# Kernel tuning notes

Hardware: AMD Instinct MI355X
Metric: run time of the kernel (lower is better)

## Reference

```python
import jax, jax.numpy as jnp
import numpy as np
from jax import lax

B, T, H, W = 1, 8, 28, 28
DIM, NH = 768, 12
HD = DIM // NH
N = 1 + T * H * W
SCALE = HD ** -0.5
STRIDE_KV = (1, 2, 2)
EPS = 1e-5


def setup_inputs():
    key = jax.random.key(0)
    ks = jax.random.split(key, 8)
    f = jax.random.normal
    return {
        "x": f(ks[0], (B, N, DIM), jnp.float32),
        "qkv_w": f(ks[1], (3 * DIM, DIM), jnp.float32) * 0.02,
        "qkv_b": jnp.zeros((3 * DIM,), jnp.float32),
        "proj_w": f(ks[2], (DIM, DIM), jnp.float32) * 0.02,
        "proj_b": jnp.zeros((DIM,), jnp.float32),
        "pool_k_w": f(ks[3], (HD, 1, 3, 3, 3), jnp.float32) * 0.1,
        "pool_v_w": f(ks[4], (HD, 1, 3, 3, 3), jnp.float32) * 0.1,
        "norm_k_g": jnp.ones((HD,), jnp.float32),
        "norm_k_b": jnp.zeros((HD,), jnp.float32),
        "norm_v_g": jnp.ones((HD,), jnp.float32),
        "norm_v_b": jnp.zeros((HD,), jnp.float32),
        "rel_pos_h": f(ks[5], (2 * H - 1, HD), jnp.float32) * 0.02,
        "rel_pos_w": f(ks[6], (2 * W - 1, HD), jnp.float32) * 0.02,
        "rel_pos_t": f(ks[7], (2 * T - 1, HD), jnp.float32) * 0.02,
    }


def _rel_idx(qn, kn):
    # static relative-distance index table (matches cal_rel_pos_* in torch)
    qr = max(kn / qn, 1.0)
    kr = max(qn / kn, 1.0)
    d = np.arange(qn)[:, None] * qr - np.arange(kn)[None, :] * kr + (kn - 1) * kr
    return d.astype(np.int32)


def _layernorm(y, g, b):
    mu = y.mean(-1, keepdims=True)
    var = ((y - mu) ** 2).mean(-1, keepdims=True)
    return (y - mu) * lax.rsqrt(var + EPS) * g + b


def _pool(t, wker, g, b):
    # t: (B, NH, N, HD); depthwise Conv3d pooling on non-cls tokens, then LN
    cls_tok, rest = t[:, :, :1], t[:, :, 1:]
    xr = rest.reshape(B * NH, T, H, W, HD)
    ker = jnp.transpose(wker, (2, 3, 4, 1, 0))  # (kT,kH,kW,1,HD)
    y = lax.conv_general_dilated(
        xr, ker, window_strides=STRIDE_KV, padding=[(1, 1), (1, 1), (1, 1)],
        dimension_numbers=("NDHWC", "DHWIO", "NDHWC"), feature_group_count=HD)
    kt, kh, kw = y.shape[1:4]
    y = y.reshape(B, NH, kt * kh * kw, HD)
    y = jnp.concatenate([cls_tok, y], axis=2)
    return _layernorm(y, g, b), (kt, kh, kw)


def reference(x, qkv_w, qkv_b, proj_w, proj_b, pool_k_w, pool_v_w,
              norm_k_g, norm_k_b, norm_v_g, norm_v_b,
              rel_pos_h, rel_pos_w, rel_pos_t):
    qkv = (x @ qkv_w.T + qkv_b).reshape(B, N, 3, NH, HD)
    qkv = jnp.transpose(qkv, (2, 0, 3, 1, 4))  # (3, B, NH, N, HD)
    q, k, v = qkv[0], qkv[1], qkv[2]
    k, (kt, kh, kw) = _pool(k, pool_k_w, norm_k_g, norm_k_b)
    v, _ = _pool(v, pool_v_w, norm_v_g, norm_v_b)

    attn = jnp.einsum("bhqc,bhkc->bhqk", q * SCALE, k)  # (B,NH,N,1+kt*kh*kw)

    # decomposed relative position bias (spatial h/w + temporal), cls excluded
    r_q = q[:, :, 1:].reshape(B, NH, T, H, W, HD)
    Rh = rel_pos_h[_rel_idx(H, kh)]  # (H, kh, HD)
    Rw = rel_pos_w[_rel_idx(W, kw)]  # (W, kw, HD)
    Rt = rel_pos_t[_rel_idx(T, kt)]  # (T, kt, HD)
    rel_h = jnp.einsum("bnthwc,hkc->bnthwk", r_q, Rh)
    rel_w = jnp.einsum("bnthwc,wkc->bnthwk", r_q, Rw)
    rel_t = jnp.einsum("bnthwc,tkc->bnthwk", r_q, Rt)
    bias = (rel_h[:, :, :, :, :, None, :, None]
            + rel_w[:, :, :, :, :, None, None, :]
            + rel_t[:, :, :, :, :, :, None, None])
    a_sp = attn[:, :, 1:, 1:].reshape(B, NH, T, H, W, kt, kh, kw) + bias
    attn = attn.at[:, :, 1:, 1:].set(a_sp.reshape(B, NH, T * H * W, kt * kh * kw))

    attn = jax.nn.softmax(attn, axis=-1)
    out = jnp.einsum("bhqk,bhkc->bhqc", attn, v)
    out = out.transpose(0, 2, 1, 3).reshape(B, N, DIM)
    return out @ proj_w.T + proj_b
```

## Files before the change

### kernel.cpp

```cpp
#include <hip/hip_runtime.h>

#define N_Q   6273
#define N_KEY 1569
#define NHEAD 12
#define HD    64
#define DQH   128
#define DIMM  768
#define NSP   6272
#define SCALE 0.125f
#define LOG2E 1.44269504f
#define QSC   (SCALE * LOG2E)
#define EPSLN 1e-5f
#define DEFER_THR 11.5f

typedef __bf16 bf16x8 __attribute__((ext_vector_type(8)));
typedef float  f32x4  __attribute__((ext_vector_type(4)));
typedef unsigned short ushort_t;
typedef unsigned int uint_t;

__device__ __forceinline__ ushort_t f2bf(float f) {
    union { float f; unsigned u; } v; v.f = f;
    unsigned r = (v.u + 0x7FFFu + ((v.u >> 16) & 1u)) >> 16;
    return (ushort_t)r;
}
__device__ __forceinline__ float bf2f(ushort_t b) {
    union { unsigned u; float f; } v; v.u = ((unsigned)b) << 16;
    return v.f;
}
__device__ __forceinline__ ushort_t cvt_native(float f) {
    __bf16 h = (__bf16)f;
    return *(ushort_t*)&h;
}
__device__ __forceinline__ uint_t pk2(float a, float b) {
    return (uint_t)cvt_native(a) | ((uint_t)cvt_native(b) << 16);
}
__device__ __forceinline__ void gload_lds16(const ushort_t* g, ushort_t* l) {
    __builtin_amdgcn_global_load_lds(
        (const __attribute__((address_space(1))) void*)g,
        (__attribute__((address_space(3))) void*)l, 16, 0, 0);
}
__device__ __forceinline__ int xcd_swz(int orig, int nwg) {
    int xcd = orig & 7, j = orig >> 3;
    int q = nwg >> 3, r = nwg & 7;
    return (xcd < r ? xcd * (q + 1) : r * (q + 1) + (xcd - r) * q) + j;
}

__global__ __launch_bounds__(256) void cvt3_bf16(
    const float* __restrict__ s0, const float* __restrict__ s1,
    const float* __restrict__ s2, ushort_t* __restrict__ dst,
    int n0, int n1, int n2)
{
    int total = n0 + n1 + n2;
    int stride = gridDim.x * 256;
    for (int i = blockIdx.x * 256 + threadIdx.x; i < total; i += stride) {
        const float* src; int j;
        if (i < n0)           { src = s0; j = i; }
        else if (i < n0 + n1) { src = s1; j = i - n0; }
        else                  { src = s2; j = i - n0 - n1; }
        const float4* s4 = (const float4*)src + (size_t)j * 2;
        float4 a = s4[0], b = s4[1];
        uint4 o;
        o.x = (unsigned)f2bf(a.x) | ((unsigned)f2bf(a.y) << 16);
        o.y = (unsigned)f2bf(a.z) | ((unsigned)f2bf(a.w) << 16);
        o.z = (unsigned)f2bf(b.x) | ((unsigned)f2bf(b.y) << 16);
        o.w = (unsigned)f2bf(b.z) | ((unsigned)f2bf(b.w) << 16);
        *(uint4*)&dst[(size_t)i * 8] = o;
    }
}

template <int MODE>
__global__ __launch_bounds__(512) void gemm_pipe(
    const ushort_t* __restrict__ A, const ushort_t* __restrict__ B,
    const float* __restrict__ bias, int M,
    float* __restrict__ Cf, ushort_t* __restrict__ qd, ushort_t* __restrict__ kd,
    ushort_t* __restrict__ vd)
{
    __shared__ ushort_t sm[32768];
    const int tid = threadIdx.x;
    const int wave = tid >> 6, lane = tid & 63;
    const int lo = lane & 15, hi = lane >> 4;
    const int nbx = gridDim.x;
    const int lin = xcd_swz(blockIdx.x + blockIdx.y * nbx, nbx * gridDim.y);
    const int bx = lin % nbx, by = lin / nbx;
    const int row0 = by * 128, col0 = bx * 128;
    const int wr = wave >> 2;
    const int wc = wave & 3;
    const int K = DIMM;
    const int NT = K / 64;

    f32x4 acc[4][2];
#pragma unroll
    for (int i = 0; i < 4; ++i)
#pragma unroll
        for (int j = 0; j < 2; ++j)
#pragma unroll
            for (int r = 0; r < 4; ++r) acc[i][j][r] = 0.f;

    const int sr = lane >> 3;
    const int scb = (lane & 7) * 16;

    auto stage = [&](int t) {
        ushort_t* Ab = sm + ((t & 1) ? 16384 : 0);
        ushort_t* Bb = Ab + 8192;
        const int k0 = t * 64;
#pragma unroll
        for (int i = 0; i < 2; ++i) {
            int ch = wave * 2 + i;
            int r = ch * 8 + sr;
            int cbs = scb ^ ((r & 7) << 4);
            int ga = row0 + r; if (ga > M - 1) ga = M - 1;
            gload_lds16(&A[(size_t)ga * K + k0 + (cbs >> 1)], &Ab[ch * 512]);
            gload_lds16(&B[(size_t)(col0 + r) * K + k0 + (cbs >> 1)], &Bb[ch * 512]);
        }
    };

    stage(0);
    for (int t = 0; t < NT; ++t) {
        __syncthreads();
        if (t + 1 < NT) stage(t + 1);
        ushort_t* Ab = sm + ((t & 1) ? 16384 : 0);
        ushort_t* Bb = Ab + 8192;
#pragma unroll
        for (int ks = 0; ks < 2; ++ks) {
            bf16x8 af[4], bfr[2];
#pragma unroll
            for (int s = 0; s < 4; ++s) {
                int ra = wr * 64 + s * 16 + lo;
                int ca = (ks * 64 + hi * 16) ^ ((ra & 7) << 4);
                af[s] = *(const bf16x8*)&Ab[ra * 64 + (ca >> 1)];
            }
#pragma unroll
            for (int s2 = 0; s2 < 2; ++s2) {
                int rb = wc * 32 + s2 * 16 + lo;
                int cb2 = (ks * 64 + hi * 16) ^ ((rb & 7) << 4);
                bfr[s2] = *(const bf16x8*)&Bb[rb * 64 + (cb2 >> 1)];
            }
#pragma unroll
            for (int i = 0; i < 4; ++i)
#pragma unroll
                for (int j = 0; j < 2; ++j)
                    acc[i][j] = __builtin_amdgcn_mfma_f32_16x16x32_bf16(
                        af[i], bfr[j], acc[i][j], 0, 0, 0);
        }
    }

#pragma unroll
    for (int i = 0; i < 4; ++i) {
#pragma unroll
        for (int reg = 0; reg < 4; ++reg) {
            int r = row0 + wr * 64 + i * 16 + hi * 4 + reg;
            if (r >= M) continue;
#pragma unroll
            for (int j = 0; j < 2; ++j) {
                int c = col0 + wc * 32 + j * 16 + lo;
                float val = acc[i][j][reg] + bias[c];
                if (MODE == 0) {
                    Cf[(size_t)r * DIMM + c] = val;
                } else {
                    int which = c / DIMM;
                    int rem = c - which * DIMM;
                    int head = rem >> 6, d = rem & 63;
                    if (which == 0) {
                        qd[((size_t)head * N_Q + r) * DQH + d] = f2bf(val * QSC);
                    } else {
                        ushort_t* dst = (which == 1) ? kd : vd;
                        dst[((size_t)head * N_Q + r) * HD + d] = f2bf(val);
                    }
                }
            }
        }
    }
}

__global__ __launch_bounds__(256) void pool_ln2(
    const ushort_t* __restrict__ kin, const ushort_t* __restrict__ vin,
    const float* __restrict__ wkk, const float* __restrict__ wkv,
    const float* __restrict__ gk, const float* __restrict__ bk,
    const float* __restrict__ gv, const float* __restrict__ bv,
    ushort_t* __restrict__ kout, ushort_t* __restrict__ vout)
{
    const int is_k = (blockIdx.y == 0);
    const ushort_t* in = is_k ? kin : vin;
    const float* wk = is_k ? wkk : wkv;
    const float* g  = is_k ? gk : gv;
    const float* b  = is_k ? bk : bv;

    __shared__ float ws_s[27][64];
    const int tid = threadIdx.x;
    for (int e = tid; e < 27 * 64; e += 256) {
        int d = e / 27, tap = e - d * 27;
        ws_s[tap][d] = wk[e];
    }
    __syncthreads();

    const int wave = tid >> 6, lane = tid & 63;
    const float gl = g[lane], bl = b[lane];

#pragma unroll 1
    for (int p4 = 0; p4 < 4; ++p4) {
        const int pos = (blockIdx.x * 4 + wave) * 4 + p4;
        if (pos >= NHEAD * N_KEY) continue;
        const int head = pos / N_KEY;
        const int idx = pos - head * N_KEY;
        const ushort_t* base = in + (size_t)head * N_Q * HD;

        float val;
        if (idx == 0) {
            val = bf2f(base[lane]);
        } else {
            int p = idx - 1;
            int t1 = p / 196;
            int h1 = (p / 14) % 14;
            int w1 = p % 14;
            val = 0.f;
            if (t1 >= 1 && t1 <= 6 && h1 >= 1 && w1 >= 1) {
                int n0 = 1 + ((t1 - 1) * 28 + (2 * h1 - 1)) * 28 + (2 * w1 - 1);
#pragma unroll
                for (int dt = 0; dt < 3; ++dt)
#pragma unroll
                    for (int dh = 0; dh < 3; ++dh)
#pragma unroll
                        for (int dw = 0; dw < 3; ++dw) {
                            int n = n0 + (dt * 784) + (dh * 28) + dw;
                            val += bf2f(base[(size_t)n * HD + lane]) *
                                   ws_s[(dt * 3 + dh) * 3 + dw][lane];
                        }
            } else {
#pragma unroll
                for (int dt = 0; dt < 3; ++dt) {
                    int t = t1 + dt - 1;
                    if (t < 0 || t >= 8) continue;
#pragma unroll
                    for (int dh = 0; dh < 3; ++dh) {
                        int h = 2 * h1 + dh - 1;
                        if (h < 0 || h >= 28) continue;
#pragma unroll
                        for (int dw = 0; dw < 3; ++dw) {
                            int w = 2 * w1 + dw - 1;
                            if (w < 0 || w >= 28) continue;
                            int n = 1 + (t * 28 + h) * 28 + w;
                            val += bf2f(base[(size_t)n * HD + lane]) *
                                   ws_s[(dt * 3 + dh) * 3 + dw][lane];
                        }
                    }
                }
            }
        }
        float mu = val;
#pragma unroll
        for (int off = 1; off < 64; off <<= 1) mu += __shfl_xor(mu, off, 64);
        mu *= (1.f / 64.f);
        float dv = val - mu;
        float var = dv * dv;
#pragma unroll
        for (int off = 1; off < 64; off <<= 1) var += __shfl_xor(var, off, 64);
        var *= (1.f / 64.f);
        float ln = dv * rsqrtf(var + EPSLN) * gl + bl;

        if (!is_k) {
            vout[(size_t)pos * HD + lane] = f2bf(ln);
        } else {
            kout[(size_t)pos * DQH + lane] = f2bf(ln);
            float oh = 0.f;
            if (idx > 0) {
                int p = idx - 1;
                int kt = p / 196, kh = (p / 14) % 14, kw = p % 14;
                if ((lane < 14 && lane == kh) ||
                    (lane >= 14 && lane < 28 && (lane - 14) == kw) ||
                    (lane >= 28 && lane < 36 && (lane - 28) == kt))
                    oh = 1.f;
            }
            kout[(size_t)pos * DQH + 64 + lane] = f2bf(oh);
        }
    }
}

__global__ __launch_bounds__(256) void rel_gemm(
    ushort_t* __restrict__ qhat, const float* __restrict__ rh,
    const float* __restrict__ rw, const float* __restrict__ rt)
{
    __shared__ ushort_t sm[17408];
    const int tid = threadIdx.x;
    const int wave = tid >> 6, lane = tid & 63;
    const int lo = lane & 15, hi = lane >> 4;
    const int head = blockIdx.y;

    if (blockIdx.x == 49) {
        if (tid < 64) qhat[((size_t)head * N_Q) * DQH + 64 + tid] = 0;
        return;
    }
    const int qs0 = blockIdx.x * 128;
    ushort_t* Al = sm;
    ushort_t* Bl = sm + 8192;

    const int sr = lane >> 3;
    const int scb = (lane & 7) * 16;
#pragma unroll
    for (int i = 0; i < 4; ++i) {
        int ch = wave * 4 + i;
        int rl = ch * 8 + sr;
        int cbs = scb ^ ((rl & 7) << 4);
        gload_lds16(&qhat[((size_t)head * N_Q + 1 + qs0 + rl) * DQH + (cbs >> 1)],
                    &Al[ch * 512]);
    }
#pragma unroll
    for (int i = 0; i < 4; ++i) {
        int u = tid + i * 256;
        int r = u >> 3, cg = u & 7;
        ushort_t tmp[8];
        if (r < 125) {
            const float* src = (r < 55) ? &rh[r * 64 + cg * 8]
                             : (r < 110) ? &rw[(r - 55) * 64 + cg * 8]
                                         : &rt[(r - 110) * 64 + cg * 8];
#pragma unroll
            for (int k = 0; k < 8; ++k) tmp[k] = f2bf(src[k]);
        } else {
#pragma unroll
            for (int k = 0; k < 8; ++k) tmp[k] = 0;
        }
        *(uint4*)&Bl[r * 64 + ((cg ^ (r & 7)) * 8)] = *(uint4*)tmp;
    }
    __syncthreads();

    f32x4 acc[2][8];
#pragma unroll
    for (int s = 0; s < 2; ++s)
#pragma unroll
        for (int cs = 0; cs < 8; ++cs)
#pragma unroll
            for (int r = 0; r < 4; ++r) acc[s][cs][r] = 0.f;

#pragma unroll
    for (int kk = 0; kk < 2; ++kk) {
        bf16x8 af[2];
#pragma unroll
        for (int s = 0; s < 2; ++s) {
            int ra = wave * 32 + s * 16 + lo;
            int ca = (kk * 32 + hi * 8) ^ ((ra & 7) * 8);
            af[s] = *(const bf16x8*)&Al[ra * 64 + ca];
        }
#pragma unroll
        for (int cs = 0; cs < 8; ++cs) {
            int rb = cs * 16 + lo;
            int cb = (kk * 32 + hi * 8) ^ ((rb & 7) * 8);
            bf16x8 bv = *(const bf16x8*)&Bl[rb * 64 + cb];
            acc[0][cs] = __builtin_amdgcn_mfma_f32_16x16x32_bf16(af[0], bv, acc[0][cs], 0, 0, 0);
            acc[1][cs] = __builtin_amdgcn_mfma_f32_16x16x32_bf16(af[1], bv, acc[1][cs], 0, 0, 0);
        }
    }
    __syncthreads();

#pragma unroll
    for (int s = 0; s < 2; ++s)
#pragma unroll
        for (int cs = 0; cs < 8; ++cs)
#pragma unroll
            for (int reg = 0; reg < 4; ++reg) {
                int rl = wave * 32 + s * 16 + hi * 4 + reg;
                sm[rl * 136 + cs * 16 + lo] = cvt_native(acc[s][cs][reg] * 8.0f);
            }
    __syncthreads();

#pragma unroll 1
    for (int it = 0; it < 18; ++it) {
        int idx = it * 64 + lane;
        int r = idx / 36;
        int j = idx - r * 36;
        int qs = qs0 + wave * 32 + r;
        int t = qs / 784, h = (qs / 28) % 28, w = qs % 28;
        int ridx;
        if (j < 14)      ridx = h - 2 * j + 26;
        else if (j < 28) ridx = 55 + (w - 2 * (j - 14) + 26);
        else             ridx = 110 + (t - (j - 28) + 7);
        ushort_t val = sm[(wave * 32 + r) * 136 + ridx];
        qhat[((size_t)head * N_Q + 1 + qs) * DQH + 64 + j] = val;
    }
}

__global__ __launch_bounds__(512) void attn_mfma(
    const ushort_t* __restrict__ qhat, const ushort_t* __restrict__ khat,
    const ushort_t* __restrict__ vp, ushort_t* __restrict__ aout)
{
    __shared__ ushort_t smem[24576];

    const int tid = threadIdx.x;
    const int wave = tid >> 6, lane = tid & 63;
    const int lo = lane & 15, hi = lane >> 4;
    const int head = blockIdx.y;
    const int q0 = xcd_swz(blockIdx.x, 50) * 128;
    const int qrow = q0 + wave * 16 + lo;

    const ushort_t* khat_h = khat + (size_t)head * N_KEY * DQH;
    const ushort_t* vp_h   = vp + (size_t)head * N_KEY * HD;

    bf16x8 qa[4];
    if (qrow < N_Q) {
        const ushort_t* qpt = &qhat[((size_t)head * N_Q + qrow) * DQH];
#pragma unroll
        for (int j = 0; j < 4; ++j) qa[j] = *(const bf16x8*)&qpt[j * 32 + hi * 8];
    } else {
#pragma unroll
        for (int j = 0; j < 4; ++j)
#pragma unroll
            for (int e = 0; e < 8; ++e) qa[j][e] = (__bf16)0.0f;
    }

    float m_run = -1e30f, l_run = 0.f;
    f32x4 o[4];
#pragma unroll
    for (int i = 0; i < 4; ++i)
#pragma unroll
        for (int r = 0; r < 4; ++r) o[i][r] = 0.f;

    const bool oddh = (hi & 1) != 0;
    const bool toph = (hi >> 1) != 0;
    const int NT = (N_KEY + 63) / 64;

    const int vkey = tid & 63, vd0 = (tid >> 6) * 8;
    uint4 vv;

    int ksrd[4][4];
#pragma unroll
    for (int kk = 0; kk < 4; ++kk)
#pragma unroll
        for (int sub = 0; sub < 4; ++sub)
            ksrd[kk][sub] = (sub * 16 + lo) * 128 + ((kk * 32 + hi * 8) ^ (lo * 8));
    int vtrd[2][4];
#pragma unroll
    for (int kh2 = 0; kh2 < 2; ++kh2)
#pragma unroll
        for (int sd = 0; sd < 4; ++sd)
            vtrd[kh2][sd] = (sd * 16 + lo) * 64 + ((kh2 * 32 + hi * 8) ^ ((lo & 7) * 8));
    int vwr[8];
#pragma unroll
    for (int j = 0; j < 8; ++j) vwr[j] = (vd0 + j) * 64 + (vkey ^ (j * 8));

    auto stage = [&](int t) {
        const int m0 = t * 64;
        ushort_t* Ksb = smem + ((t & 1) << 13);
#pragma unroll
        for (int i = 0; i < 2; ++i) {
            int ch = wave * 2 + i;
            int kr = ch * 4 + hi;
            int cb = (lo * 16) ^ ((kr & 15) << 4);
            int gm = m0 + kr; if (gm > N_KEY - 1) gm = N_KEY - 1;
            gload_lds16(&khat_h[(gm << 7) + (cb >> 1)], &Ksb[ch * 512]);
        }
        int gm = m0 + vkey; if (gm > N_KEY - 1) gm = N_KEY - 1;
        vv = *(const uint4*)&vp_h[(gm << 6) + vd0];
    };

    stage(0);
#pragma unroll 2
    for (int t = 0; t < NT; ++t) {
        const int m0 = t * 64;
        ushort_t* Ksb = smem + ((t & 1) << 13);
        ushort_t* Vtb = smem + 16384 + ((t & 1) << 12);

        {
            ushort_t tmp[8];
            *(uint4*)tmp = vv;
#pragma unroll
            for (int j = 0; j < 8; ++j) Vtb[vwr[j]] = tmp[j];
        }
        __syncthreads();
        if (t + 1 < NT) stage(t + 1);

        f32x4 s[4];
#pragma unroll
        for (int sub = 0; sub < 4; ++sub)
#pragma unroll
            for (int r = 0; r < 4; ++r) s[sub][r] = 0.f;
        __builtin_amdgcn_s_setprio(1);
#pragma unroll
        for (int kk = 0; kk < 4; ++kk) {
#pragma unroll
            for (int sub = 0; sub < 4; ++sub) {
                bf16x8 kf = *(const bf16x8*)&Ksb[ksrd[kk][sub]];
                s[sub] = __builtin_amdgcn_mfma_f32_16x16x32_bf16(kf, qa[kk], s[sub], 0, 0, 0);
            }
        }
        __builtin_amdgcn_s_setprio(0);

        if (m0 + 64 > N_KEY) {
#pragma unroll
            for (int sub = 0; sub < 4; ++sub)
#pragma unroll
                for (int reg = 0; reg < 4; ++reg)
                    if (m0 + sub * 16 + hi * 4 + reg >= N_KEY) s[sub][reg] = -1e30f;
        }

        float rm = s[0][0];
#pragma unroll
        for (int sub = 0; sub < 4; ++sub)
#pragma unroll
            for (int reg = 0; reg < 4; ++reg) rm = fmaxf(rm, s[sub][reg]);
        rm = fmaxf(rm, __shfl_xor(rm, 16));
        rm = fmaxf(rm, __shfl_xor(rm, 32));

        if (__any(rm - m_run > DEFER_THR)) {
            float mnew = fmaxf(m_run, rm);
            float corr = exp2f(m_run - mnew);
            float ps = 0.f;
#pragma unroll
            for (int sub = 0; sub < 4; ++sub)
#pragma unroll
                for (int reg = 0; reg < 4; ++reg) {
                    float pp = exp2f(s[sub][reg] - mnew);
                    s[sub][reg] = pp; ps += pp;
                }
            ps += __shfl_xor(ps, 16);
            ps += __shfl_xor(ps, 32);
            l_run = l_run * corr + ps;
            m_run = mnew;
#pragma unroll
            for (int i = 0; i < 4; ++i)
#pragma unroll
                for (int r = 0; r < 4; ++r) o[i][r] *= corr;
        } else {
            float ps = 0.f;
#pragma unroll
            for (int sub = 0; sub < 4; ++sub)
#pragma unroll
                for (int reg = 0; reg < 4; ++reg) {
                    float pp = exp2f(s[sub][reg] - m_run);
                    s[sub][reg] = pp; ps += pp;
                }
            ps += __shfl_xor(ps, 16);
            ps += __shfl_xor(ps, 32);
            l_run += ps;
        }

#pragma unroll
        for (int kh2 = 0; kh2 < 2; ++kh2) {
            uint_t x0a = pk2(s[2 * kh2][0], s[2 * kh2][1]);
            uint_t x0b = pk2(s[2 * kh2][2], s[2 * kh2][3]);
            uint_t x1a = pk2(s[2 * kh2 + 1][0], s[2 * kh2 + 1][1]);
            uint_t x1b = pk2(s[2 * kh2 + 1][2], s[2 * kh2 + 1][3]);
            uint_t y0a = __shfl_xor(x0a, 16), y0b = __shfl_xor(x0b, 16);
            uint_t y1a = __shfl_xor(x1a, 16), y1b = __shfl_xor(x1b, 16);
            uint_t c0[4] = { oddh ? y0a : x0a, oddh ? y0b : x0b,
                             oddh ? x0a : y0a, oddh ? x0b : y0b };
            uint_t c1[4] = { oddh ? y1a : x1a, oddh ? y1b : x1b,
                             oddh ? x1a : y1a, oddh ? x1b : y1b };
            union { uint_t u[4]; bf16x8 v; } pw;
#pragma unroll
            for (int i2 = 0; i2 < 4; ++i2) {
                uint_t send = oddh ? c0[i2] : c1[i2];
                uint_t f = __shfl_xor(send, 32);
                pw.u[i2] = (toph != oddh) ? f : (oddh ? c1[i2] : c0[i2]);
            }
            __builtin_amdgcn_s_setprio(1);
#pragma unroll
            for (int sub_d = 0; sub_d < 4; ++sub_d) {
                bf16x8 vf = *(const bf16x8*)&Vtb[vtrd[kh2][sub_d]];
                o[sub_d] = __builtin_amdgcn_mfma_f32_16x16x32_bf16(vf, pw.v, o[sub_d], 0, 0, 0);
            }
            __builtin_amdgcn_s_setprio(0);
        }
    }

    ushort_t* Ob = smem + wave * (16 * 88);
    __syncthreads();
    float inv = 1.f / l_run;
#pragma unroll
    for (int sub_d = 0; sub_d < 4; ++sub_d)
#pragma unroll
        for (int reg = 0; reg < 4; ++reg)
            Ob[lo * 88 + sub_d * 16 + hi * 4 + reg] = cvt_native(o[sub_d][reg] * inv);
    __syncthreads();
#pragma unroll
    for (int i = 0; i < 2; ++i) {
        int e = lane + i * 64;
        int r = e >> 3, cc = e & 7;
        int gq = q0 + wave * 16 + r;
        if (gq < N_Q) {
            uint4 ov = *(const uint4*)&Ob[r * 88 + cc * 8];
            *(uint4*)&aout[(size_t)gq * DIMM + head * HD + cc * 8] = ov;
        }
    }
}

extern "C" void kernel_launch(void* const* d_in, const int* in_sizes, int n_in,
                              void* d_out, int out_size, void* d_ws, size_t ws_size,
                              hipStream_t stream)
{
    const float* x      = (const float*)d_in[0];
    const float* qkv_w  = (const float*)d_in[1];
    const float* qkv_b  = (const float*)d_in[2];
    const float* proj_w = (const float*)d_in[3];
    const float* proj_b = (const float*)d_in[4];
    const float* pkw    = (const float*)d_in[5];
    const float* pvw    = (const float*)d_in[6];
    const float* nkg    = (const float*)d_in[7];
    const float* nkb    = (const float*)d_in[8];
    const float* nvg    = (const float*)d_in[9];
    const float* nvb    = (const float*)d_in[10];
    const float* rph    = (const float*)d_in[11];
    const float* rpw    = (const float*)d_in[12];
    const float* rpt    = (const float*)d_in[13];

    const size_t SZ_X     = (size_t)N_Q * DIMM;
    const size_t SZ_QKVW  = (size_t)3 * DIMM * DIMM;
    const size_t SZ_PROJW = (size_t)DIMM * DIMM;
    const size_t SZ_QHAT  = (size_t)NHEAD * N_Q * DQH;
    const size_t SZ_KV    = (size_t)NHEAD * N_Q * HD;
    const size_t SZ_KHAT  = (size_t)NHEAD * N_KEY * DQH;
    const size_t SZ_VPO   = (size_t)NHEAD * N_KEY * HD;

    ushort_t* xb     = (ushort_t*)d_ws;
    ushort_t* qkvwb  = xb + SZ_X;
    ushort_t* projwb = qkvwb + SZ_QKVW;
    ushort_t* qhat   = projwb + SZ_PROJW;
    ushort_t* kb     = qhat + SZ_QHAT;
    ushort_t* vb     = kb + SZ_KV;
    ushort_t* khat   = vb + SZ_KV;
    ushort_t* vpo    = khat + SZ_KHAT;
    ushort_t* aout   = vpo + SZ_VPO;
    float*    outp   = (float*)d_out;

    cvt3_bf16<<<2048, 256, 0, stream>>>(x, qkv_w, proj_w, xb,
                                        (int)(SZ_X / 8), (int)(SZ_QKVW / 8),
                                        (int)(SZ_PROJW / 8));
    gemm_pipe<1><<<dim3(18, 50), 512, 0, stream>>>(xb, qkvwb, qkv_b, N_Q,
                                                   nullptr, qhat, kb, vb);
    pool_ln2<<<dim3((NHEAD * N_KEY + 15) / 16, 2), 256, 0, stream>>>(
        kb, vb, pkw, pvw, nkg, nkb, nvg, nvb, khat, vpo);
    rel_gemm<<<dim3(50, NHEAD), 256, 0, stream>>>(qhat, rph, rpw, rpt);
    attn_mfma<<<dim3((N_Q + 127) / 128, NHEAD), 512, 0, stream>>>(
        qhat, khat, vpo, aout);
    gemm_pipe<0><<<dim3(6, 50), 512, 0, stream>>>(aout, projwb, proj_b, N_Q,
                                                  outp, nullptr, nullptr, nullptr);
}
```

Baseline: 257.6 us.

## Fuse relative-position GEMM into attention prologue and shrink Q storage

Removes the separate rel_gemm kernel. Each attention wave now computes its own query rows' projections onto the relative-position tables with MFMA in LDS and gathers them into the extra Q columns in registers. Q is stored with head dim 64 instead of a padded 128, which halves Q writes in the QKV GEMM and drops a read-modify-write pass. The cost is extra prologue work and an LDS staging step with two barriers in every attention block, and the rel tables are converted once per block.

```diff
diff --git a/kernel.cpp b/kernel.cpp
--- a/kernel.cpp
+++ b/kernel.cpp
@@ -161,7 +161,7 @@
                     int rem = c - which * DIMM;
                     int head = rem >> 6, d = rem & 63;
                     if (which == 0) {
-                        qd[((size_t)head * N_Q + r) * DQH + d] = f2bf(val * QSC);
+                        qd[((size_t)head * N_Q + r) * HD + d] = f2bf(val * QSC);
                     } else {
                         ushort_t* dst = (which == 1) ? kd : vd;
                         dst[((size_t)head * N_Q + r) * HD + d] = f2bf(val);
@@ -275,111 +275,11 @@
     }
 }
 
-__global__ __launch_bounds__(256) void rel_gemm(
-    ushort_t* __restrict__ qhat, const float* __restrict__ rh,
-    const float* __restrict__ rw, const float* __restrict__ rt)
-{
-    __shared__ ushort_t sm[17408];
-    const int tid = threadIdx.x;
-    const int wave = tid >> 6, lane = tid & 63;
-    const int lo = lane & 15, hi = lane >> 4;
-    const int head = blockIdx.y;
-
-    if (blockIdx.x == 49) {
-        if (tid < 64) qhat[((size_t)head * N_Q) * DQH + 64 + tid] = 0;
-        return;
-    }
-    const int qs0 = blockIdx.x * 128;
-    ushort_t* Al = sm;
-    ushort_t* Bl = sm + 8192;
-
-    const int sr = lane >> 3;
-    const int scb = (lane & 7) * 16;
-#pragma unroll
-    for (int i = 0; i < 4; ++i) {
-        int ch = wave * 4 + i;
-        int rl = ch * 8 + sr;
-        int cbs = scb ^ ((rl & 7) << 4);
-        gload_lds16(&qhat[((size_t)head * N_Q + 1 + qs0 + rl) * DQH + (cbs >> 1)],
-                    &Al[ch * 512]);
-    }
-#pragma unroll
-    for (int i = 0; i < 4; ++i) {
-        int u = tid + i * 256;
-        int r = u >> 3, cg = u & 7;
-        ushort_t tmp[8];
-        if (r < 125) {
-            const float* src = (r < 55) ? &rh[r * 64 + cg * 8]
-                             : (r < 110) ? &rw[(r - 55) * 64 + cg * 8]
-                                         : &rt[(r - 110) * 64 + cg * 8];
-#pragma unroll
-            for (int k = 0; k < 8; ++k) tmp[k] = f2bf(src[k]);
-        } else {
-#pragma unroll
-            for (int k = 0; k < 8; ++k) tmp[k] = 0;
-        }
-        *(uint4*)&Bl[r * 64 + ((cg ^ (r & 7)) * 8)] = *(uint4*)tmp;
-    }
-    __syncthreads();
-
-    f32x4 acc[2][8];
-#pragma unroll
-    for (int s = 0; s < 2; ++s)
-#pragma unroll
-        for (int cs = 0; cs < 8; ++cs)
-#pragma unroll
-            for (int r = 0; r < 4; ++r) acc[s][cs][r] = 0.f;
-
-#pragma unroll
-    for (int kk = 0; kk < 2; ++kk) {
-        bf16x8 af[2];
-#pragma unroll
-        for (int s = 0; s < 2; ++s) {
-            int ra = wave * 32 + s * 16 + lo;
-            int ca = (kk * 32 + hi * 8) ^ ((ra & 7) * 8);
-            af[s] = *(const bf16x8*)&Al[ra * 64 + ca];
-        }
-#pragma unroll
-        for (int cs = 0; cs < 8; ++cs) {
-            int rb = cs * 16 + lo;
-            int cb = (kk * 32 + hi * 8) ^ ((rb & 7) * 8);
-            bf16x8 bv = *(const bf16x8*)&Bl[rb * 64 + cb];
-            acc[0][cs] = __builtin_amdgcn_mfma_f32_16x16x32_bf16(af[0], bv, acc[0][cs], 0, 0, 0);
-            acc[1][cs] = __builtin_amdgcn_mfma_f32_16x16x32_bf16(af[1], bv, acc[1][cs], 0, 0, 0);
-        }
-    }
-    __syncthreads();
-
-#pragma unroll
-    for (int s = 0; s < 2; ++s)
-#pragma unroll
-        for (int cs = 0; cs < 8; ++cs)
-#pragma unroll
-            for (int reg = 0; reg < 4; ++reg) {
-                int rl = wave * 32 + s * 16 + hi * 4 + reg;
-                sm[rl * 136 + cs * 16 + lo] = cvt_native(acc[s][cs][reg] * 8.0f);
-            }
-    __syncthreads();
-
-#pragma unroll 1
-    for (int it = 0; it < 18; ++it) {
-        int idx = it * 64 + lane;
-        int r = idx / 36;
-        int j = idx - r * 36;
-        int qs = qs0 + wave * 32 + r;
-        int t = qs / 784, h = (qs / 28) % 28, w = qs % 28;
-        int ridx;
-        if (j < 14)      ridx = h - 2 * j + 26;
-        else if (j < 28) ridx = 55 + (w - 2 * (j - 14) + 26);
-        else             ridx = 110 + (t - (j - 28) + 7);
-        ushort_t val = sm[(wave * 32 + r) * 136 + ridx];
-        qhat[((size_t)head * N_Q + 1 + qs) * DQH + 64 + j] = val;
-    }
-}
-
 __global__ __launch_bounds__(512) void attn_mfma(
     const ushort_t* __restrict__ qhat, const ushort_t* __restrict__ khat,
-    const ushort_t* __restrict__ vp, ushort_t* __restrict__ aout)
+    const ushort_t* __restrict__ vp,
+    const float* __restrict__ rh, const float* __restrict__ rw,
+    const float* __restrict__ rt, ushort_t* __restrict__ aout)
 {
     __shared__ ushort_t smem[24576];
 
@@ -395,14 +295,87 @@
 
     bf16x8 qa[4];
     if (qrow < N_Q) {
-        const ushort_t* qpt = &qhat[((size_t)head * N_Q + qrow) * DQH];
-#pragma unroll
-        for (int j = 0; j < 4; ++j) qa[j] = *(const bf16x8*)&qpt[j * 32 + hi * 8];
+        const ushort_t* qpt = &qhat[((size_t)head * N_Q + qrow) * HD];
+        qa[0] = *(const bf16x8*)&qpt[hi * 8];
+        qa[1] = *(const bf16x8*)&qpt[32 + hi * 8];
     } else {
 #pragma unroll
-        for (int j = 0; j < 4; ++j)
+        for (int j = 0; j < 2; ++j)
 #pragma unroll
             for (int e = 0; e < 8; ++e) qa[j][e] = (__bf16)0.0f;
+    }
+
+    {
+        ushort_t* Rl = smem + 16384;
+        ushort_t* Gb = smem;
+#pragma unroll
+        for (int i = 0; i < 2; ++i) {
+            int u = tid + i * 512;
+            int r = u >> 3, cg = u & 7;
+            ushort_t tmp[8];
+            if (r < 125) {
+                const float* src = (r < 55) ? &rh[r * 64 + cg * 8]
+                                 : (r < 110) ? &rw[(r - 55) * 64 + cg * 8]
+                                             : &rt[(r - 110) * 64 + cg * 8];
+#pragma unroll
+                for (int k2 = 0; k2 < 8; ++k2) tmp[k2] = f2bf(src[k2]);
+            } else {
+#pragma unroll
+                for (int k2 = 0; k2 < 8; ++k2) tmp[k2] = 0;
+            }
+            *(uint4*)&Rl[r * 64 + cg * 8] = *(uint4*)tmp;
+        }
+        __syncthreads();
+
+        ushort_t* Gw = Gb + wave * 2048;
+#pragma unroll
+        for (int half = 0; half < 2; ++half) {
+            f32x4 gac[4];
+#pragma unroll
+            for (int c4 = 0; c4 < 4; ++c4)
+#pragma unroll
+                for (int r = 0; r < 4; ++r) gac[c4][r] = 0.f;
+#pragma unroll
+            for (int kk = 0; kk < 2; ++kk)
+#pragma unroll
+                for (int c4 = 0; c4 < 4; ++c4) {
+                    int cs = half * 4 + c4;
+                    bf16x8 bv = *(const bf16x8*)&Rl[(cs * 16 + lo) * 64 +
+                                                    kk * 32 + hi * 8];
+                    gac[c4] = __builtin_amdgcn_mfma_f32_16x16x32_bf16(
+                        qa[kk], bv, gac[c4], 0, 0, 0);
+                }
+#pragma unroll
+            for (int c4 = 0; c4 < 4; ++c4)
+#pragma unroll
+                for (int reg = 0; reg < 4; ++reg) {
+                    int cs = half * 4 + c4;
+                    Gw[(hi * 4 + reg) * 128 + cs * 16 + lo] =
+                        cvt_native(gac[c4][reg] * 8.0f);
+                }
+        }
+        const ushort_t* Gme = &Gw[lo * 128];
+        int qs = qrow - 1;
+        int tq = qs / 784, hq = (qs / 28) % 28, wq = qs % 28;
+        bool rowok = (qrow >= 1 && qrow < N_Q);
+        union { ushort_t u16[8]; bf16x8 v; } q2, q3;
+#pragma unroll
+        for (int e = 0; e < 8; ++e) {
+            int j2 = hi * 8 + e;
+            int ridx = (j2 < 14) ? (hq - 2 * j2 + 26)
+                     : (j2 < 28) ? (55 + (wq - 2 * (j2 - 14) + 26))
+                                 : (110 + (tq - (j2 - 28) + 7));
+            q2.u16[e] = rowok ? Gme[ridx] : (ushort_t)0;
+            if (hi == 0 && e < 4) {
+                int j3 = 32 + e;
+                int r3 = 110 + (tq - (j3 - 28) + 7);
+                q3.u16[e] = rowok ? Gme[r3] : (ushort_t)0;
+            } else {
+                q3.u16[e] = 0;
+            }
+        }
+        qa[2] = q2.v; qa[3] = q3.v;
+        __syncthreads();
     }
 
     float m_run = -1e30f, l_run = 0.f;
@@ -603,7 +576,6 @@
     const size_t SZ_X     = (size_t)N_Q * DIMM;
     const size_t SZ_QKVW  = (size_t)3 * DIMM * DIMM;
     const size_t SZ_PROJW = (size_t)DIMM * DIMM;
-    const size_t SZ_QHAT  = (size_t)NHEAD * N_Q * DQH;
     const size_t SZ_KV    = (size_t)NHEAD * N_Q * HD;
     const size_t SZ_KHAT  = (size_t)NHEAD * N_KEY * DQH;
     const size_t SZ_VPO   = (size_t)NHEAD * N_KEY * HD;
@@ -612,7 +584,7 @@
     ushort_t* qkvwb  = xb + SZ_X;
     ushort_t* projwb = qkvwb + SZ_QKVW;
     ushort_t* qhat   = projwb + SZ_PROJW;
-    ushort_t* kb     = qhat + SZ_QHAT;
+    ushort_t* kb     = qhat + SZ_KV;
     ushort_t* vb     = kb + SZ_KV;
     ushort_t* khat   = vb + SZ_KV;
     ushort_t* vpo    = khat + SZ_KHAT;
@@ -626,9 +598,8 @@
                                                    nullptr, qhat, kb, vb);
     pool_ln2<<<dim3((NHEAD * N_KEY + 15) / 16, 2), 256, 0, stream>>>(
         kb, vb, pkw, pvw, nkg, nkb, nvg, nvb, khat, vpo);
-    rel_gemm<<<dim3(50, NHEAD), 256, 0, stream>>>(qhat, rph, rpw, rpt);
     attn_mfma<<<dim3((N_Q + 127) / 128, NHEAD), 512, 0, stream>>>(
-        qhat, khat, vpo, aout);
+        qhat, khat, vpo, rph, rpw, rpt, aout);
     gemm_pipe<0><<<dim3(6, 50), 512, 0, stream>>>(aout, projwb, proj_b, N_Q,
                                                   outp, nullptr, nullptr, nullptr);
 }
```

Result: slower. 275.6 us (+7.0%).
